# Kernel optimization log

Measured on AMD Instinct MI355X. Metric: run time of the kernel, lower is better.

The kernel has to match this reference:

```python
import jax, jax.numpy as jnp
import numpy as np

N_NODES, NUM_GRAPHS, MAX_N = 65536, 512, 192
D, H = 512, 8
DH = D // H


def setup_inputs() -> dict:
    key = jax.random.key(0)
    ks = jax.random.split(key, 13)
    s = 1.0 / np.sqrt(D).astype(np.float32)
    return {
        "node_features": jax.random.normal(ks[0], (N_NODES, D), jnp.float32),
        "batch_indices": jnp.sort(jax.random.randint(ks[1], (N_NODES,), 0, NUM_GRAPHS)),
        "global_query": jax.random.normal(ks[2], (1, H, 1, DH), jnp.float32) * s,
        "w_q": jax.random.normal(ks[3], (D, D), jnp.float32) * s,
        "b_q": jax.random.normal(ks[4], (D,), jnp.float32) * 0.02,
        "w_k": jax.random.normal(ks[5], (D, D), jnp.float32) * s,
        "b_k": jax.random.normal(ks[6], (D,), jnp.float32) * 0.02,
        "w_v": jax.random.normal(ks[7], (D, D), jnp.float32) * s,
        "b_v": jax.random.normal(ks[8], (D,), jnp.float32) * 0.02,
        "w_o": jax.random.normal(ks[9], (D, D), jnp.float32) * s,
        "b_o": jax.random.normal(ks[10], (D,), jnp.float32) * 0.02,
        "w_p": jax.random.normal(ks[11], (D, D), jnp.float32) * s,
        "b_p": jax.random.normal(ks[12], (D,), jnp.float32) * 0.02,
    }


def reference(node_features, batch_indices, global_query, w_q, b_q, w_k, b_k,
              w_v, b_v, w_o, b_o, w_p, b_p):
    # ragged bookkeeping (batch_indices is sorted)
    counts = jax.ops.segment_sum(jnp.ones_like(batch_indices), batch_indices,
                                 num_segments=NUM_GRAPHS)            # [G]
    offsets = jnp.cumsum(counts) - counts                            # [G]
    pos = jnp.arange(N_NODES) - offsets[batch_indices]               # local node pos

    # pad nodes to dense [G, MAX_N, D]
    dense = jnp.zeros((NUM_GRAPHS, MAX_N, D), node_features.dtype)
    dense = dense.at[batch_indices, pos].set(node_features)
    mask = jnp.zeros((NUM_GRAPHS, MAX_N), bool).at[batch_indices, pos].set(True)

    # Faithful replication of torch's expand+reshape of global_query:
    # Q_in[g, t, d] = gq_flat[h*DH + d%DH] with h = (t*D + d) // (n_g*DH)
    gqf = global_query.reshape(H * DH)
    t = jnp.arange(MAX_N)[:, None]                                   # [MAX_N,1]
    d = jnp.arange(D)[None, :]                                       # [1,D]
    n = jnp.maximum(counts, 1)[:, None, None]                        # [G,1,1]
    h = jnp.clip((t * D + d)[None] // (n * DH), 0, H - 1)            # [G,MAX_N,D]
    q_in = gqf[h * DH + (d % DH)[None]]                              # [G,MAX_N,D]

    Q = (q_in @ w_q.T + b_q).reshape(NUM_GRAPHS, MAX_N, H, DH)
    K = (dense @ w_k.T + b_k).reshape(NUM_GRAPHS, MAX_N, H, DH)
    V = (dense @ w_v.T + b_v).reshape(NUM_GRAPHS, MAX_N, H, DH)

    scale = 1.0 / np.sqrt(DH).astype(np.float32)
    scores = jnp.einsum('gthd,gshd->ghts', Q, K) * scale             # [G,H,T,S]
    scores = jnp.where(mask[:, None, None, :], scores, -1e9)
    attn_w = jax.nn.softmax(scores, axis=-1)
    attn = jnp.einsum('ghts,gshd->gthd', attn_w, V).reshape(NUM_GRAPHS, MAX_N, D)
    attn = attn @ w_o.T + b_o

    denom = jnp.maximum(counts, 1).astype(attn.dtype)[:, None]
    pooled = (attn * mask[..., None].astype(attn.dtype)).sum(axis=1) / denom
    return jax.nn.relu(pooled @ w_p.T + b_p)                         # [G, D]
```

## Files before the change

kernel.cpp:

```cpp
#include <hip/hip_runtime.h>
#include <hip/hip_bf16.h>
#include <cstdint>

typedef __bf16 bf16;
typedef __attribute__((ext_vector_type(8))) __bf16 bf16x8;
typedef __attribute__((ext_vector_type(4))) __bf16 bf16x4;
typedef __attribute__((ext_vector_type(2))) __bf16 bf16x2;
typedef __attribute__((ext_vector_type(4))) float f32x4;

#define N_NODES    65536
#define NUM_GRAPHS 512
#define MAX_N      192
#define D          512
#define H          8
#define DH         64
#define UMAX       64
#define USTRIDE    132

__device__ __forceinline__ void gload_lds16(const void* g, void* l) {
    __builtin_amdgcn_global_load_lds((const __attribute__((address_space(1))) void*)g,
                                     (__attribute__((address_space(3))) void*)l, 16, 0, 0);
}

__global__ __launch_bounds__(256) void lb_kernel(const int* __restrict__ batch,
                                                 int* __restrict__ lb) {
    int g = blockIdx.x * 256 + threadIdx.x;
    if (g > NUM_GRAPHS) return;
    int lo = 0, hi = N_NODES;
    while (lo < hi) {
        int mid = (lo + hi) >> 1;
        if (batch[mid] < g) lo = mid + 1; else hi = mid;
    }
    lb[g] = lo;
}

__global__ __launch_bounds__(192) void dedup_kernel(const int* __restrict__ lb,
                                                    int* __restrict__ udata) {
    const int g = blockIdx.x;
    const int off = lb[g];
    const int n = min(lb[g + 1] - off, MAX_N);
    __shared__ int keys[MAX_N];
    const int t = threadIdx.x;
    if (t < n) {
        unsigned un = (unsigned)n;
        int key = 0;
        #pragma unroll
        for (int p = 0; p < 8; p++) key |= (int)(((unsigned)(8 * t + p)) / un) << (3 * p);
        keys[t] = key;
    }
    __syncthreads();
    if (t == 0) {
        int* base = udata + (size_t)g * USTRIDE;
        int nu = 0;
        for (int s = 0; s < n; s++) {
            if (s == 0 || keys[s] != keys[s - 1]) {
                if (nu < UMAX) { base[1 + nu] = keys[s]; base[65 + nu] = 0; nu++; }
            }
            base[65 + (nu - 1)] += 1;
        }
        base[0] = nu;
    }
}

__global__ __launch_bounds__(256) void cvt_kernel(const float* __restrict__ src,
                                                  bf16* __restrict__ dst, int n) {
    int i = (blockIdx.x * 256 + threadIdx.x) * 4;
    if (i >= n) return;
    float4 v = *(const float4*)(src + i);
    bf16x4 o = {(bf16)v.x, (bf16)v.y, (bf16)v.z, (bf16)v.w};
    *(bf16x4*)(dst + i) = o;
}

__global__ __launch_bounds__(256) void p2_kernel(const float* __restrict__ gq,
                                                 const float* __restrict__ wq,
                                                 float* __restrict__ P2) {
    int h = blockIdx.x, p = blockIdx.y;
    __shared__ float gs[64];
    if (threadIdx.x < 64) gs[threadIdx.x] = gq[h * 64 + threadIdx.x];
    __syncthreads();
    for (int o = threadIdx.x; o < D; o += 256) {
        const float* wr = wq + (size_t)o * D + p * 64;
        float acc = 0.f;
        #pragma unroll 16
        for (int j = 0; j < 64; j++) acc += gs[j] * wr[j];
        P2[(size_t)(h * 8 + p) * D + o] = acc;
    }
}

__global__ __launch_bounds__(256) void wov_kernel(const float* __restrict__ wo,
                                                  const float* __restrict__ wv,
                                                  bf16* __restrict__ Wov) {
    const int ot = blockIdx.x;
    const int h  = blockIdx.y;
    __shared__ float wos[32 * 64];
    for (int idx = threadIdx.x; idx < 32 * 64; idx += 256) {
        int ol = idx >> 6, j = idx & 63;
        wos[idx] = wo[(size_t)(ot * 32 + ol) * D + h * 64 + j];
    }
    __syncthreads();
    const int c = threadIdx.x * 2;
    float acc0[32] = {}, acc1[32] = {};
    for (int j = 0; j < 64; j++) {
        float2 v2 = *(const float2*)(wv + (size_t)(h * 64 + j) * D + c);
        #pragma unroll
        for (int o = 0; o < 32; o++) {
            float wj = wos[o * 64 + j];
            acc0[o] += wj * v2.x; acc1[o] += wj * v2.y;
        }
    }
    #pragma unroll
    for (int o = 0; o < 32; o++) {
        bf16x2 r = {(bf16)acc0[o], (bf16)acc1[o]};
        *(bf16x2*)(Wov + (size_t)(ot * 32 + o) * 4096 + h * 512 + c) = r;
    }
}

__global__ __launch_bounds__(256) void cst_kernel(const float* __restrict__ wo,
                                                  const float* __restrict__ bv,
                                                  const float* __restrict__ bo,
                                                  float* __restrict__ cst) {
    int o = blockIdx.x * 256 + threadIdx.x;
    if (o >= D) return;
    const float* wr = wo + (size_t)o * D;
    float acc = bo[o];
    for (int d0 = 0; d0 < D; d0 += 4) {
        float4 wv4 = *(const float4*)(wr + d0);
        float4 b4  = *(const float4*)(bv + d0);
        acc += wv4.x * b4.x + wv4.y * b4.y + wv4.z * b4.z + wv4.w * b4.w;
    }
    cst[o] = acc;
}

__global__ __launch_bounds__(256) void k_gemm(const bf16* __restrict__ Ab,
                                              const bf16* __restrict__ Wkb,
                                              const float* __restrict__ bkb,
                                              bf16* __restrict__ Kout) {
    const int i0 = blockIdx.x * 128;
    const int o0 = blockIdx.y * 128;
    __shared__ bf16 As[128 * 32];
    __shared__ bf16 Bs[128 * 32];
    const int tid = threadIdx.x;
    const int lane = tid & 63;
    const int w = tid >> 6;
    const int wm = w & 1, wn = w >> 1;
    const int fr = lane & 15, quad = lane >> 4;
    const bf16* gA = Ab + (size_t)(i0 + w * 32 + (lane >> 2)) * D + (lane & 3) * 8;
    const bf16* gB = Wkb + (size_t)(o0 + w * 32 + (lane >> 2)) * D + (lane & 3) * 8;
    bf16* lA = As + (w * 32) * 32;
    bf16* lB = Bs + (w * 32) * 32;

    f32x4 acc[4][4] = {};

    for (int kt = 0; kt < D; kt += 32) {
        __syncthreads();
        gload_lds16(gA + kt, lA);
        gload_lds16(gA + (size_t)16 * D + kt, lA + 16 * 32);
        gload_lds16(gB + kt, lB);
        gload_lds16(gB + (size_t)16 * D + kt, lB + 16 * 32);
        __syncthreads();
        bf16x8 fa[4], fb[4];
        #pragma unroll
        for (int mf = 0; mf < 4; mf++)
            fa[mf] = *(const bf16x8*)(As + (wm * 64 + mf * 16 + fr) * 32 + quad * 8);
        #pragma unroll
        for (int nf = 0; nf < 4; nf++)
            fb[nf] = *(const bf16x8*)(Bs + (wn * 64 + nf * 16 + fr) * 32 + quad * 8);
        #pragma unroll
        for (int mf = 0; mf < 4; mf++)
            #pragma unroll
            for (int nf = 0; nf < 4; nf++)
                acc[mf][nf] = __builtin_amdgcn_mfma_f32_16x16x32_bf16(fa[mf], fb[nf], acc[mf][nf], 0, 0, 0);
    }
    #pragma unroll
    for (int nf = 0; nf < 4; nf++) {
        const int col = o0 + wn * 64 + nf * 16 + fr;
        const float bs = bkb[col];
        #pragma unroll
        for (int mf = 0; mf < 4; mf++) {
            const int row = i0 + wm * 64 + mf * 16 + quad * 4;
            #pragma unroll
            for (int r = 0; r < 4; r++)
                Kout[(size_t)(row + r) * D + col] = (bf16)(acc[mf][nf][r] + bs);
        }
    }
}

__global__ __launch_bounds__(256) void attn_kernel(const bf16* __restrict__ Kb,
                                                   const float* __restrict__ P2,
                                                   const float* __restrict__ bq,
                                                   const int* __restrict__ lb,
                                                   const int* __restrict__ udata,
                                                   float* __restrict__ Wbar) {
    const int g = blockIdx.y;
    const int tid = threadIdx.x;
    const int lane = tid & 63;
    const int w = tid >> 6;
    const int h = blockIdx.x * 4 + w;
    const int off = lb[g];
    const int n = min(lb[g + 1] - off, MAX_N);

    __shared__ bf16 Qs[4][16 * 80];
    __shared__ float wacc[4][MAX_N];
    __shared__ int upat_l[UMAX], ucnt_l[UMAX];

    const int* ubase = udata + (size_t)g * USTRIDE;
    const int nu = ubase[0];
    if (tid < 64) {
        upat_l[tid] = (tid < nu) ? ubase[1 + tid] : 0;
        ucnt_l[tid] = (tid < nu) ? ubase[65 + tid] : 0;
    }
    wacc[w][lane] = 0.f; wacc[w][64 + lane] = 0.f; wacc[w][128 + lane] = 0.f;
    __syncthreads();

    if (n == 0) return;

    const int fr = lane & 15;
    const int quad = lane >> 4;
    const float inv_n = 1.0f / (float)n;

    for (int c0 = 0; c0 < nu; c0 += 16) {
        {
            const int ul = lane >> 2;
            const int j0 = (lane & 3) * 16;
            const bool valid = (c0 + ul) < nu;
            const int pat = upat_l[c0 + ul];
            const float* bpq = bq + h * 64 + j0;
            float4 q0 = *(const float4*)bpq;
            float4 q1 = *(const float4*)(bpq + 4);
            float4 q2 = *(const float4*)(bpq + 8);
            float4 q3 = *(const float4*)(bpq + 12);
            #pragma unroll
            for (int p = 0; p < 8; p++) {
                const int hp = (pat >> (3 * p)) & 7;
                const float* pp = P2 + (size_t)(hp * 8 + p) * D + h * 64 + j0;
                float4 t0 = *(const float4*)pp;
                float4 t1 = *(const float4*)(pp + 4);
                float4 t2 = *(const float4*)(pp + 8);
                float4 t3 = *(const float4*)(pp + 12);
                q0.x += t0.x; q0.y += t0.y; q0.z += t0.z; q0.w += t0.w;
                q1.x += t1.x; q1.y += t1.y; q1.z += t1.z; q1.w += t1.w;
                q2.x += t2.x; q2.y += t2.y; q2.z += t2.z; q2.w += t2.w;
                q3.x += t3.x; q3.y += t3.y; q3.z += t3.z; q3.w += t3.w;
            }
            if (!valid) {
                q0.x=q0.y=q0.z=q0.w=0.f; q1.x=q1.y=q1.z=q1.w=0.f;
                q2.x=q2.y=q2.z=q2.w=0.f; q3.x=q3.y=q3.z=q3.w=0.f;
            }
            bf16x8 b0 = {(bf16)q0.x,(bf16)q0.y,(bf16)q0.z,(bf16)q0.w,
                         (bf16)q1.x,(bf16)q1.y,(bf16)q1.z,(bf16)q1.w};
            bf16x8 b1 = {(bf16)q2.x,(bf16)q2.y,(bf16)q2.z,(bf16)q2.w,
                         (bf16)q3.x,(bf16)q3.y,(bf16)q3.z,(bf16)q3.w};
            *(bf16x8*)(&Qs[w][ul * 80 + j0])     = b0;
            *(bf16x8*)(&Qs[w][ul * 80 + j0 + 8]) = b1;
        }
        bf16x8 fa0 = *(const bf16x8*)(&Qs[w][fr * 80 + quad * 8]);
        bf16x8 fa1 = *(const bf16x8*)(&Qs[w][fr * 80 + 32 + quad * 8]);

        f32x4 sc[12];
        #pragma unroll
        for (int st = 0; st < 12; st++) {
            if (st * 16 < n) {
                int s = st * 16 + fr;
                int row = off + (s < n ? s : n - 1);
                const bf16* kp = Kb + (size_t)row * D + h * 64 + quad * 8;
                bf16x8 fb0 = *(const bf16x8*)kp;
                bf16x8 fb1 = *(const bf16x8*)(kp + 32);
                f32x4 a = {0.f, 0.f, 0.f, 0.f};
                a = __builtin_amdgcn_mfma_f32_16x16x32_bf16(fa0, fb0, a, 0, 0, 0);
                a = __builtin_amdgcn_mfma_f32_16x16x32_bf16(fa1, fb1, a, 0, 0, 0);
                if (s < n) {
                    sc[st].x = a.x * 0.125f; sc[st].y = a.y * 0.125f;
                    sc[st].z = a.z * 0.125f; sc[st].w = a.w * 0.125f;
                } else {
                    sc[st].x = sc[st].y = sc[st].z = sc[st].w = -1e30f;
                }
            } else {
                sc[st].x = sc[st].y = sc[st].z = sc[st].w = -1e30f;
            }
        }
        float m[4] = {-1e30f, -1e30f, -1e30f, -1e30f};
        #pragma unroll
        for (int st = 0; st < 12; st++) {
            m[0] = fmaxf(m[0], sc[st].x); m[1] = fmaxf(m[1], sc[st].y);
            m[2] = fmaxf(m[2], sc[st].z); m[3] = fmaxf(m[3], sc[st].w);
        }
        #pragma unroll
        for (int o = 1; o <= 8; o <<= 1) {
            #pragma unroll
            for (int r = 0; r < 4; r++) m[r] = fmaxf(m[r], __shfl_xor(m[r], o));
        }
        float den[4] = {0.f, 0.f, 0.f, 0.f};
        #pragma unroll
        for (int st = 0; st < 12; st++) {
            float e0 = __expf(sc[st].x - m[0]); float e1 = __expf(sc[st].y - m[1]);
            float e2 = __expf(sc[st].z - m[2]); float e3 = __expf(sc[st].w - m[3]);
            sc[st].x = e0; sc[st].y = e1; sc[st].z = e2; sc[st].w = e3;
            den[0] += e0; den[1] += e1; den[2] += e2; den[3] += e3;
        }
        #pragma unroll
        for (int o = 1; o <= 8; o <<= 1) {
            #pragma unroll
            for (int r = 0; r < 4; r++) den[r] += __shfl_xor(den[r], o);
        }
        float wf[4];
        #pragma unroll
        for (int r = 0; r < 4; r++)
            wf[r] = (float)ucnt_l[c0 + quad * 4 + r] * inv_n / den[r];
        #pragma unroll
        for (int st = 0; st < 12; st++) {
            float v = sc[st].x * wf[0] + sc[st].y * wf[1] + sc[st].z * wf[2] + sc[st].w * wf[3];
            v += __shfl_xor(v, 16);
            v += __shfl_xor(v, 32);
            if (lane < 16) wacc[w][st * 16 + lane] += v;
        }
    }
    for (int s = lane; s < n; s += 64)
        Wbar[(size_t)h * N_NODES + off + s] = wacc[w][s];
}

__global__ __launch_bounds__(256) void abar_kernel(const float* __restrict__ A,
                                                   const float* __restrict__ Wbar,
                                                   const int* __restrict__ lb,
                                                   bf16* __restrict__ abar) {
    const int g = blockIdx.x;
    const int off = lb[g];
    const int n = min(lb[g + 1] - off, MAX_N);
    const int tid = threadIdx.x;
    bf16* outg = abar + (size_t)g * 4096;
    if (n == 0) {
        bf16x2 z = {(bf16)0.f, (bf16)0.f};
        for (int idx = tid; idx < 2048; idx += 256) *(bf16x2*)(outg + idx * 2) = z;
        return;
    }
    __shared__ float wsh[MAX_N * 8];
    for (int idx = tid; idx < n * 8; idx += 256) {
        int s = idx >> 3, h = idx & 7;
        wsh[idx] = Wbar[(size_t)h * N_NODES + off + s];
    }
    __syncthreads();
    const int c = tid * 2;
    float acc0[8] = {}, acc1[8] = {};
    for (int s = 0; s < n; s++) {
        float2 a2 = *(const float2*)(A + (size_t)(off + s) * D + c);
        const float* wp_ = wsh + s * 8;
        #pragma unroll
        for (int h = 0; h < 8; h++) {
            acc0[h] += wp_[h] * a2.x;
            acc1[h] += wp_[h] * a2.y;
        }
    }
    #pragma unroll
    for (int h = 0; h < 8; h++) {
        bf16x2 r = {(bf16)acc0[h], (bf16)acc1[h]};
        *(bf16x2*)(outg + h * 512 + c) = r;
    }
}

__global__ __launch_bounds__(256) void zero_kernel(float* __restrict__ p, int n4) {
    int i = blockIdx.x * 256 + threadIdx.x;
    if (i < n4) { float4 z = {0.f, 0.f, 0.f, 0.f}; *(float4*)(p + i * 4) = z; }
}

__global__ __launch_bounds__(256) void og_gemm(const bf16* __restrict__ Ab,
                                               const bf16* __restrict__ Bb,
                                               float* __restrict__ Yt) {
    const int o0 = blockIdx.x * 128;
    const int i0 = blockIdx.y * 128;
    const int k0 = blockIdx.z * 512;
    __shared__ bf16 As[128 * 32];
    __shared__ bf16 Bs[128 * 32];
    const int tid = threadIdx.x;
    const int lane = tid & 63;
    const int w = tid >> 6;
    const int wm = w & 1, wn = w >> 1;
    const int fr = lane & 15, quad = lane >> 4;
    const bf16* gA = Ab + (size_t)(i0 + w * 32 + (lane >> 2)) * 4096 + k0 + (lane & 3) * 8;
    const bf16* gB = Bb + (size_t)(o0 + w * 32 + (lane >> 2)) * 4096 + k0 + (lane & 3) * 8;
    bf16* lA = As + (w * 32) * 32;
    bf16* lB = Bs + (w * 32) * 32;

    f32x4 acc[4][4] = {};

    for (int kt = 0; kt < 512; kt += 32) {
        __syncthreads();
        gload_lds16(gA + kt, lA);
        gload_lds16(gA + (size_t)16 * 4096 + kt, lA + 16 * 32);
        gload_lds16(gB + kt, lB);
        gload_lds16(gB + (size_t)16 * 4096 + kt, lB + 16 * 32);
        __syncthreads();
        bf16x8 fa[4], fb[4];
        #pragma unroll
        for (int mf = 0; mf < 4; mf++)
            fa[mf] = *(const bf16x8*)(As + (wm * 64 + mf * 16 + fr) * 32 + quad * 8);
        #pragma unroll
        for (int nf = 0; nf < 4; nf++)
            fb[nf] = *(const bf16x8*)(Bs + (wn * 64 + nf * 16 + fr) * 32 + quad * 8);
        #pragma unroll
        for (int mf = 0; mf < 4; mf++)
            #pragma unroll
            for (int nf = 0; nf < 4; nf++)
                acc[mf][nf] = __builtin_amdgcn_mfma_f32_16x16x32_bf16(fa[mf], fb[nf], acc[mf][nf], 0, 0, 0);
    }
    #pragma unroll
    for (int nf = 0; nf < 4; nf++) {
        const int col = o0 + wn * 64 + nf * 16 + fr;
        #pragma unroll
        for (int mf = 0; mf < 4; mf++) {
            const int row = i0 + wm * 64 + mf * 16 + quad * 4;
            #pragma unroll
            for (int r = 0; r < 4; r++)
                atomicAdd(&Yt[(size_t)(row + r) * D + col], acc[mf][nf][r]);
        }
    }
}

__global__ __launch_bounds__(256) void proj_p(const float* __restrict__ tmp,
                                              const float* __restrict__ cst,
                                              const bf16* __restrict__ Wpb,
                                              const float* __restrict__ bp,
                                              const int* __restrict__ lb,
                                              float* __restrict__ out) {
    const int o0 = blockIdx.x * 128;
    const int i0 = blockIdx.y * 128;
    __shared__ bf16 As[128 * 32];
    __shared__ bf16 Bs[128 * 32];
    const int tid = threadIdx.x;
    const int lane = tid & 63;
    const int w = tid >> 6;
    const int wm = w & 1, wn = w >> 1;
    const int fr = lane & 15, quad = lane >> 4;
    const int ar = tid >> 1;
    const int ac = (tid & 1) * 16;
    const int g = i0 + ar;
    const bool live = lb[g + 1] - lb[g] > 0;
    const float* tp = tmp + (size_t)g * D + ac;
    const float* cp = cst + ac;
    const bf16* gB = Wpb + (size_t)(o0 + w * 32 + (lane >> 2)) * D + (lane & 3) * 8;
    bf16* lB = Bs + (w * 32) * 32;

    f32x4 acc[4][4] = {};

    for (int kt = 0; kt < D; kt += 32) {
        __syncthreads();
        gload_lds16(gB + kt, lB);
        gload_lds16(gB + (size_t)16 * D + kt, lB + 16 * 32);
        {
            float4 x0 = *(const float4*)(tp + kt);
            float4 x1 = *(const float4*)(tp + kt + 4);
            float4 x2 = *(const float4*)(tp + kt + 8);
            float4 x3 = *(const float4*)(tp + kt + 12);
            float4 c0 = *(const float4*)(cp + kt);
            float4 c1 = *(const float4*)(cp + kt + 4);
            float4 c2 = *(const float4*)(cp + kt + 8);
            float4 c3 = *(const float4*)(cp + kt + 12);
            float s = live ? 1.f : 0.f;
            bf16x8 v0 = {(bf16)((x0.x+c0.x)*s),(bf16)((x0.y+c0.y)*s),(bf16)((x0.z+c0.z)*s),(bf16)((x0.w+c0.w)*s),
                         (bf16)((x1.x+c1.x)*s),(bf16)((x1.y+c1.y)*s),(bf16)((x1.z+c1.z)*s),(bf16)((x1.w+c1.w)*s)};
            bf16x8 v1 = {(bf16)((x2.x+c2.x)*s),(bf16)((x2.y+c2.y)*s),(bf16)((x2.z+c2.z)*s),(bf16)((x2.w+c2.w)*s),
                         (bf16)((x3.x+c3.x)*s),(bf16)((x3.y+c3.y)*s),(bf16)((x3.z+c3.z)*s),(bf16)((x3.w+c3.w)*s)};
            *(bf16x8*)(As + ar * 32 + ac) = v0;
            *(bf16x8*)(As + ar * 32 + ac + 8) = v1;
        }
        __syncthreads();
        bf16x8 fa[4], fb[4];
        #pragma unroll
        for (int mf = 0; mf < 4; mf++)
            fa[mf] = *(const bf16x8*)(As + (wm * 64 + mf * 16 + fr) * 32 + quad * 8);
        #pragma unroll
        for (int nf = 0; nf < 4; nf++)
            fb[nf] = *(const bf16x8*)(Bs + (wn * 64 + nf * 16 + fr) * 32 + quad * 8);
        #pragma unroll
        for (int mf = 0; mf < 4; mf++)
            #pragma unroll
            for (int nf = 0; nf < 4; nf++)
                acc[mf][nf] = __builtin_amdgcn_mfma_f32_16x16x32_bf16(fa[mf], fb[nf], acc[mf][nf], 0, 0, 0);
    }
    #pragma unroll
    for (int nf = 0; nf < 4; nf++) {
        const int col = o0 + wn * 64 + nf * 16 + fr;
        const float bs = bp[col];
        #pragma unroll
        for (int mf = 0; mf < 4; mf++) {
            const int row = i0 + wm * 64 + mf * 16 + quad * 4;
            #pragma unroll
            for (int r = 0; r < 4; r++)
                out[(size_t)(row + r) * D + col] = fmaxf(acc[mf][nf][r] + bs, 0.f);
        }
    }
}

extern "C" void kernel_launch(void* const* d_in, const int* in_sizes, int n_in,
                              void* d_out, int out_size, void* d_ws, size_t ws_size,
                              hipStream_t stream) {
    const float* nf    = (const float*)d_in[0];
    const int*   batch = (const int*)d_in[1];
    const float* gq    = (const float*)d_in[2];
    const float* wq    = (const float*)d_in[3];
    const float* bq    = (const float*)d_in[4];
    const float* wk    = (const float*)d_in[5];
    const float* bk    = (const float*)d_in[6];
    const float* wv    = (const float*)d_in[7];
    const float* bv    = (const float*)d_in[8];
    const float* wo    = (const float*)d_in[9];
    const float* bo    = (const float*)d_in[10];
    const float* wp    = (const float*)d_in[11];
    const float* bp    = (const float*)d_in[12];
    float* out = (float*)d_out;

    char* ws = (char*)d_ws;
    bf16*  Abf  = (bf16*)ws;
    float* Wbar = (float*)ws;
    bf16*  abar = (bf16*)(ws + ((size_t)2 << 20));
    bf16*  Wov  = (bf16*)(ws + ((size_t)6 << 20));
    float* tmp  = (float*)(ws + ((size_t)10 << 20));
    float* cst  = (float*)(ws + ((size_t)11 << 20));
    bf16*  Kb   = (bf16*)(ws + ((size_t)64 << 20));
    char* sm = ws + ((size_t)128 << 20);
    int*  lb    = (int*)sm;    sm += 4096;
    int*  udata = (int*)sm;    sm += (size_t)NUM_GRAPHS * USTRIDE * 4 + 2048;
    bf16* Wkb   = (bf16*)sm;   sm += (size_t)D * D * 2;
    bf16* Wpb   = (bf16*)sm;   sm += (size_t)D * D * 2;
    float* P2   = (float*)sm;  sm += (size_t)64 * D * 4;

    lb_kernel<<<3, 256, 0, stream>>>(batch, lb);
    dedup_kernel<<<NUM_GRAPHS, 192, 0, stream>>>(lb, udata);
    cvt_kernel<<<(D * D / 4) / 256, 256, 0, stream>>>(wk, Wkb, D * D);
    cvt_kernel<<<(D * D / 4) / 256, 256, 0, stream>>>(wp, Wpb, D * D);
    p2_kernel<<<dim3(8, 8), 256, 0, stream>>>(gq, wq, P2);
    cvt_kernel<<<(N_NODES * D / 4) / 256, 256, 0, stream>>>(nf, Abf, N_NODES * D);
    k_gemm<<<dim3(N_NODES / 128, 4), 256, 0, stream>>>(Abf, Wkb, bk, Kb);
    wov_kernel<<<dim3(16, 8), 256, 0, stream>>>(wo, wv, Wov);
    cst_kernel<<<2, 256, 0, stream>>>(wo, bv, bo, cst);
    attn_kernel<<<dim3(2, NUM_GRAPHS), 256, 0, stream>>>(Kb, P2, bq, lb, udata, Wbar);
    abar_kernel<<<NUM_GRAPHS, 256, 0, stream>>>(nf, Wbar, lb, abar);
    zero_kernel<<<(NUM_GRAPHS * D / 4 + 255) / 256, 256, 0, stream>>>(tmp, NUM_GRAPHS * D / 4);
    og_gemm<<<dim3(4, 4, 8), 256, 0, stream>>>(abar, Wov, tmp);
    proj_p<<<dim3(4, 4), 256, 0, stream>>>(tmp, cst, Wpb, bp, lb, out);
}
```

Before: 446.9 us.

## Fuse fp32-to-bf16 conversion into K GEMM and abar reduction into attention

The separate conversion pass over node features goes away. The K GEMM now reads fp32 features, converts them to bf16 in registers and writes them to LDS, and its epilogue is staged through shared memory so global stores are coalesced 16-byte rows. The attention kernel now runs all 8 heads per graph in one 512-thread block and computes the weighted feature sum (abar) directly from its shared weights. That removes the Wbar round trip and the abar_kernel launch. The trade-offs are twice the A-operand load bytes in the GEMM, loss of async LDS loads for A, and heavier blocks with more shared memory in the attention kernel.

```diff
diff --git a/kernel.cpp b/kernel.cpp
--- a/kernel.cpp
+++ b/kernel.cpp
@@ -131,32 +131,43 @@
     cst[o] = acc;
 }
 
-__global__ __launch_bounds__(256) void k_gemm(const bf16* __restrict__ Ab,
+__global__ __launch_bounds__(256) void k_gemm(const float* __restrict__ Af,
                                               const bf16* __restrict__ Wkb,
                                               const float* __restrict__ bkb,
                                               bf16* __restrict__ Kout) {
     const int i0 = blockIdx.x * 128;
     const int o0 = blockIdx.y * 128;
-    __shared__ bf16 As[128 * 32];
-    __shared__ bf16 Bs[128 * 32];
+    __shared__ char smem[64 * 132 * 2];
+    bf16* As = (bf16*)smem;
+    bf16* Bs = (bf16*)(smem + 8192);
     const int tid = threadIdx.x;
     const int lane = tid & 63;
     const int w = tid >> 6;
     const int wm = w & 1, wn = w >> 1;
     const int fr = lane & 15, quad = lane >> 4;
-    const bf16* gA = Ab + (size_t)(i0 + w * 32 + (lane >> 2)) * D + (lane & 3) * 8;
-    const bf16* gB = Wkb + (size_t)(o0 + w * 32 + (lane >> 2)) * D + (lane & 3) * 8;
-    bf16* lA = As + (w * 32) * 32;
+    const int sr = lane >> 2;
+    const int sc = (lane & 3) * 8;
+    const float* gA = Af + (size_t)(i0 + w * 32 + sr) * D + sc;
+    const bf16*  gB = Wkb + (size_t)(o0 + w * 32 + sr) * D + sc;
+    bf16* lA = As + (w * 32 + sr) * 32 + sc;
     bf16* lB = Bs + (w * 32) * 32;
 
     f32x4 acc[4][4] = {};
 
     for (int kt = 0; kt < D; kt += 32) {
-        __syncthreads();
-        gload_lds16(gA + kt, lA);
-        gload_lds16(gA + (size_t)16 * D + kt, lA + 16 * 32);
+        float4 a0 = *(const float4*)(gA + kt);
+        float4 a1 = *(const float4*)(gA + kt + 4);
+        float4 a2 = *(const float4*)(gA + (size_t)16 * D + kt);
+        float4 a3 = *(const float4*)(gA + (size_t)16 * D + kt + 4);
+        __syncthreads();
         gload_lds16(gB + kt, lB);
         gload_lds16(gB + (size_t)16 * D + kt, lB + 16 * 32);
+        bf16x8 wA0 = {(bf16)a0.x,(bf16)a0.y,(bf16)a0.z,(bf16)a0.w,
+                      (bf16)a1.x,(bf16)a1.y,(bf16)a1.z,(bf16)a1.w};
+        bf16x8 wA1 = {(bf16)a2.x,(bf16)a2.y,(bf16)a2.z,(bf16)a2.w,
+                      (bf16)a3.x,(bf16)a3.y,(bf16)a3.z,(bf16)a3.w};
+        *(bf16x8*)lA = wA0;
+        *(bf16x8*)(lA + 16 * 32) = wA1;
         __syncthreads();
         bf16x8 fa[4], fb[4];
         #pragma unroll
@@ -171,37 +182,62 @@
             for (int nf = 0; nf < 4; nf++)
                 acc[mf][nf] = __builtin_amdgcn_mfma_f32_16x16x32_bf16(fa[mf], fb[nf], acc[mf][nf], 0, 0, 0);
     }
+
+    bf16* Cs = (bf16*)smem;
     #pragma unroll
-    for (int nf = 0; nf < 4; nf++) {
-        const int col = o0 + wn * 64 + nf * 16 + fr;
-        const float bs = bkb[col];
-        #pragma unroll
-        for (int mf = 0; mf < 4; mf++) {
-            const int row = i0 + wm * 64 + mf * 16 + quad * 4;
-            #pragma unroll
-            for (int r = 0; r < 4; r++)
-                Kout[(size_t)(row + r) * D + col] = (bf16)(acc[mf][nf][r] + bs);
-        }
-    }
-}
-
-__global__ __launch_bounds__(256) void attn_kernel(const bf16* __restrict__ Kb,
+    for (int pass = 0; pass < 2; pass++) {
+        __syncthreads();
+        if (wm == pass) {
+            #pragma unroll
+            for (int nf = 0; nf < 4; nf++) {
+                const int col = wn * 64 + nf * 16 + fr;
+                const float bs = bkb[o0 + col];
+                #pragma unroll
+                for (int mf = 0; mf < 4; mf++) {
+                    #pragma unroll
+                    for (int r = 0; r < 4; r++)
+                        Cs[(mf * 16 + quad * 4 + r) * 132 + col] = (bf16)(acc[mf][nf][r] + bs);
+                }
+            }
+        }
+        __syncthreads();
+        #pragma unroll
+        for (int k = 0; k < 4; k++) {
+            int idx = k * 256 + tid;
+            int row = idx >> 4;
+            int coff = (idx & 15) * 8;
+            bf16x8 v = *(const bf16x8*)(Cs + row * 132 + coff);
+            *(bf16x8*)(Kout + (size_t)(i0 + pass * 64 + row) * D + o0 + coff) = v;
+        }
+    }
+}
+
+__global__ __launch_bounds__(512) void attn_kernel(const bf16* __restrict__ Kb,
                                                    const float* __restrict__ P2,
                                                    const float* __restrict__ bq,
                                                    const int* __restrict__ lb,
                                                    const int* __restrict__ udata,
-                                                   float* __restrict__ Wbar) {
-    const int g = blockIdx.y;
+                                                   const float* __restrict__ Af,
+                                                   bf16* __restrict__ abar) {
+    const int g = blockIdx.x;
     const int tid = threadIdx.x;
     const int lane = tid & 63;
     const int w = tid >> 6;
-    const int h = blockIdx.x * 4 + w;
+    const int h = w;
     const int off = lb[g];
     const int n = min(lb[g + 1] - off, MAX_N);
 
-    __shared__ bf16 Qs[4][16 * 80];
-    __shared__ float wacc[4][MAX_N];
+    __shared__ bf16 Qs[8][16 * 80];
+    __shared__ float wacc[8][MAX_N];
     __shared__ int upat_l[UMAX], ucnt_l[UMAX];
+
+    bf16* outg = abar + (size_t)g * 4096;
+    if (n == 0) {
+        const bf16 z0 = (bf16)0.f;
+        bf16x8 z = {z0, z0, z0, z0, z0, z0, z0, z0};
+        *(bf16x8*)(outg + tid * 8) = z;
+        return;
+    }
 
     const int* ubase = udata + (size_t)g * USTRIDE;
     const int nu = ubase[0];
@@ -211,8 +247,6 @@
     }
     wacc[w][lane] = 0.f; wacc[w][64 + lane] = 0.f; wacc[w][128 + lane] = 0.f;
     __syncthreads();
-
-    if (n == 0) return;
 
     const int fr = lane & 15;
     const int quad = lane >> 4;
@@ -314,46 +348,24 @@
             if (lane < 16) wacc[w][st * 16 + lane] += v;
         }
     }
-    for (int s = lane; s < n; s += 64)
-        Wbar[(size_t)h * N_NODES + off + s] = wacc[w][s];
-}
-
-__global__ __launch_bounds__(256) void abar_kernel(const float* __restrict__ A,
-                                                   const float* __restrict__ Wbar,
-                                                   const int* __restrict__ lb,
-                                                   bf16* __restrict__ abar) {
-    const int g = blockIdx.x;
-    const int off = lb[g];
-    const int n = min(lb[g + 1] - off, MAX_N);
-    const int tid = threadIdx.x;
-    bf16* outg = abar + (size_t)g * 4096;
-    if (n == 0) {
-        bf16x2 z = {(bf16)0.f, (bf16)0.f};
-        for (int idx = tid; idx < 2048; idx += 256) *(bf16x2*)(outg + idx * 2) = z;
-        return;
-    }
-    __shared__ float wsh[MAX_N * 8];
-    for (int idx = tid; idx < n * 8; idx += 256) {
-        int s = idx >> 3, h = idx & 7;
-        wsh[idx] = Wbar[(size_t)h * N_NODES + off + s];
-    }
+
     __syncthreads();
-    const int c = tid * 2;
-    float acc0[8] = {}, acc1[8] = {};
+    const int cp = lane * 8;
+    const float* Ag = Af + (size_t)off * D + cp;
+    const float* wp_ = wacc[w];
+    float acc0[8] = {};
     for (int s = 0; s < n; s++) {
-        float2 a2 = *(const float2*)(A + (size_t)(off + s) * D + c);
-        const float* wp_ = wsh + s * 8;
-        #pragma unroll
-        for (int h = 0; h < 8; h++) {
-            acc0[h] += wp_[h] * a2.x;
-            acc1[h] += wp_[h] * a2.y;
-        }
-    }
-    #pragma unroll
-    for (int h = 0; h < 8; h++) {
-        bf16x2 r = {(bf16)acc0[h], (bf16)acc1[h]};
-        *(bf16x2*)(outg + h * 512 + c) = r;
-    }
+        float4 x0 = *(const float4*)(Ag + (size_t)s * D);
+        float4 x1 = *(const float4*)(Ag + (size_t)s * D + 4);
+        float wv = wp_[s];
+        acc0[0] += wv * x0.x; acc0[1] += wv * x0.y;
+        acc0[2] += wv * x0.z; acc0[3] += wv * x0.w;
+        acc0[4] += wv * x1.x; acc0[5] += wv * x1.y;
+        acc0[6] += wv * x1.z; acc0[7] += wv * x1.w;
+    }
+    bf16x8 r = {(bf16)acc0[0],(bf16)acc0[1],(bf16)acc0[2],(bf16)acc0[3],
+                (bf16)acc0[4],(bf16)acc0[5],(bf16)acc0[6],(bf16)acc0[7]};
+    *(bf16x8*)(outg + h * 512 + cp) = r;
 }
 
 __global__ __launch_bounds__(256) void zero_kernel(float* __restrict__ p, int n4) {
@@ -508,8 +520,6 @@
     float* out = (float*)d_out;
 
     char* ws = (char*)d_ws;
-    bf16*  Abf  = (bf16*)ws;
-    float* Wbar = (float*)ws;
     bf16*  abar = (bf16*)(ws + ((size_t)2 << 20));
     bf16*  Wov  = (bf16*)(ws + ((size_t)6 << 20));
     float* tmp  = (float*)(ws + ((size_t)10 << 20));
@@ -527,12 +537,10 @@
     cvt_kernel<<<(D * D / 4) / 256, 256, 0, stream>>>(wk, Wkb, D * D);
     cvt_kernel<<<(D * D / 4) / 256, 256, 0, stream>>>(wp, Wpb, D * D);
     p2_kernel<<<dim3(8, 8), 256, 0, stream>>>(gq, wq, P2);
-    cvt_kernel<<<(N_NODES * D / 4) / 256, 256, 0, stream>>>(nf, Abf, N_NODES * D);
-    k_gemm<<<dim3(N_NODES / 128, 4), 256, 0, stream>>>(Abf, Wkb, bk, Kb);
+    k_gemm<<<dim3(N_NODES / 128, 4), 256, 0, stream>>>(nf, Wkb, bk, Kb);
     wov_kernel<<<dim3(16, 8), 256, 0, stream>>>(wo, wv, Wov);
     cst_kernel<<<2, 256, 0, stream>>>(wo, bv, bo, cst);
-    attn_kernel<<<dim3(2, NUM_GRAPHS), 256, 0, stream>>>(Kb, P2, bq, lb, udata, Wbar);
-    abar_kernel<<<NUM_GRAPHS, 256, 0, stream>>>(nf, Wbar, lb, abar);
+    attn_kernel<<<NUM_GRAPHS, 512, 0, stream>>>(Kb, P2, bq, lb, udata, nf, abar);
     zero_kernel<<<(NUM_GRAPHS * D / 4 + 255) / 256, 256, 0, stream>>>(tmp, NUM_GRAPHS * D / 4);
     og_gemm<<<dim3(4, 4, 8), 256, 0, stream>>>(abar, Wov, tmp);
     proj_p<<<dim3(4, 4), 256, 0, stream>>>(tmp, cst, Wpb, bp, lb, out);
```

After: 460.3 us. 3.0% more time.
